# Performance work log

Hardware: AMD Instinct MI355X
Metric: run time of the kernel (lower is better)

The kernel has to match this reference:

```python
import jax, jax.numpy as jnp
import numpy as np

H = 16        # num_attention_heads
DH = 64       # attention_head_dim
D = H * DH    # model dim = 1024
FF = 4 * D    # feed-forward inner dim = 4096
SCALE = DH ** -0.5
EPS = 1e-12


def _ln(x, g, b):
    m = jnp.mean(x, axis=-1, keepdims=True)
    v = jnp.mean((x - m) ** 2, axis=-1, keepdims=True)
    return (x - m) * jax.lax.rsqrt(v + EPS) * g + b


def _attn(x, ctx, Wq, Wk, Wv, Wo, bo, mask):
    # x: [B,S,D] (already pre-normed), ctx: [B,T,D], mask: [B,T] int (1=keep) or None
    B, S, _ = x.shape
    T = ctx.shape[1]
    q = (x @ Wq).reshape(B, S, H, DH)
    k = (ctx @ Wk).reshape(B, T, H, DH)
    v = (ctx @ Wv).reshape(B, T, H, DH)
    scores = jnp.einsum('bqhd,bkhd->bhqk', q, k) * SCALE  # [B,H,S,T]
    if mask is not None:
        scores = jnp.where(mask[:, None, None, :] == 0, -jnp.inf, scores)
    probs = jax.nn.softmax(scores, axis=-1)
    out = jnp.einsum('bhqk,bkhd->bqhd', probs, v).reshape(B, S, D)
    return out @ Wo + bo


def _geglu_ff(x, Wff1, bff1, Wff2, bff2):
    y = x @ Wff1 + bff1                 # [B,S,2*FF]
    h, gate = y[..., :FF], y[..., FF:]
    # GEGLU computes exact (erf) gelu in fp32
    g = jax.nn.gelu(gate.astype(jnp.float32), approximate=False).astype(gate.dtype)
    return (h * g) @ Wff2 + bff2


def setup_inputs() -> dict:
    key = jax.random.key(0)
    ks = jax.random.split(key, 24)
    B, S, T = 4, 1024, 1024
    w = lambda k, shp: jax.random.normal(k, shp, dtype=jnp.float32) * 0.02
    inp = {
        'hidden_states': jax.random.normal(ks[0], (B, S, D), dtype=jnp.float32),
        'context': jax.random.normal(ks[1], (B, T, D), dtype=jnp.float32),
        'encoder_key_padding_mask': jnp.ones((B, T), dtype=jnp.int32),
        'g1': jnp.ones((D,), jnp.float32), 'b1': jnp.zeros((D,), jnp.float32),
        'g2': jnp.ones((D,), jnp.float32), 'b2': jnp.zeros((D,), jnp.float32),
        'g3': jnp.ones((D,), jnp.float32), 'b3': jnp.zeros((D,), jnp.float32),
        'Wq1': w(ks[2], (D, D)), 'Wk1': w(ks[3], (D, D)), 'Wv1': w(ks[4], (D, D)),
        'Wo1': w(ks[5], (D, D)), 'bo1': jnp.zeros((D,), jnp.float32),
        'Wq2': w(ks[6], (D, D)), 'Wk2': w(ks[7], (D, D)), 'Wv2': w(ks[8], (D, D)),
        'Wo2': w(ks[9], (D, D)), 'bo2': jnp.zeros((D,), jnp.float32),
        'Wff1': w(ks[10], (D, 2 * FF)), 'bff1': jnp.zeros((2 * FF,), jnp.float32),
        'Wff2': w(ks[11], (FF, D)), 'bff2': jnp.zeros((D,), jnp.float32),
    }
    return inp


def reference(hidden_states, context, encoder_key_padding_mask,
              g1, b1, g2, b2, g3, b3,
              Wq1, Wk1, Wv1, Wo1, bo1,
              Wq2, Wk2, Wv2, Wo2, bo2,
              Wff1, bff1, Wff2, bff2):
    # Self-attention (attn1): context defaults to (normed) hidden_states, no padding mask
    n1 = _ln(hidden_states, g1, b1)
    h = hidden_states + _attn(n1, n1, Wq1, Wk1, Wv1, Wo1, bo1, None)
    # Cross-attention (attn2) with encoder key padding mask
    n2 = _ln(h, g2, b2)
    h = h + _attn(n2, context, Wq2, Wk2, Wv2, Wo2, bo2, encoder_key_padding_mask)
    # GEGLU feed-forward
    h = h + _geglu_ff(_ln(h, g3, b3), Wff1, bff1, Wff2, bff2)
    return h
```

## Files before the change

kernel.cpp:

```cpp
#include <hip/hip_runtime.h>

typedef unsigned short u16;
typedef unsigned int u32;

#define B_ 4
#define S_ 1024
#define D_ 1024
#define H_ 16
#define DH_ 64
#define FF_ 4096
#define M_ 4096
#define SCALE_ 0.125f

typedef __attribute__((ext_vector_type(8))) __bf16 bf16x8;
typedef __attribute__((ext_vector_type(4))) float f32x4;

__device__ __forceinline__ f32x4 mfma16(bf16x8 a, bf16x8 b, f32x4 c) {
  return __builtin_amdgcn_mfma_f32_16x16x32_bf16(a, b, c, 0, 0, 0);
}

__device__ __forceinline__ u16 f2bf(float x) {
  union { __bf16 h; u16 u; } cv; cv.h = (__bf16)x; return cv.u;
}
__device__ __forceinline__ float bf2f(u16 u) {
  union { u32 u; float f; } cv; cv.u = ((u32)u) << 16; return cv.f;
}
__device__ __forceinline__ u32 packbf2(float a, float b) {
  union { u32 u; __bf16 h[2]; } pk;
  pk.h[0] = (__bf16)a; pk.h[1] = (__bf16)b;
  return pk.u;
}
__device__ __forceinline__ float gelu_exact(float x) {
  return 0.5f * x * (1.f + erff(x * 0.7071067811865475f));
}
__device__ __forceinline__ void gload16(const void* g, void* l) {
  __builtin_amdgcn_global_load_lds((__attribute__((address_space(1))) void*)(g),
                                   (__attribute__((address_space(3))) void*)(l),
                                   16, 0, 0);
}

template<int EPI>
__global__ __launch_bounds__(256, 2) void gemm128(
    const u16* __restrict__ A, const u16* __restrict__ BT,
    const float* __restrict__ bias, const float* __restrict__ res,
    const u16* __restrict__ aux, void* __restrict__ out,
    int M, int N, int K, int ktiles)
{
  __shared__ u16 As[2][128 * 64];
  __shared__ u16 Bs[2][128 * 64];

  const int tid = threadIdx.x;
  const int wave = tid >> 6, lane = tid & 63;
  const int wm = wave >> 1, wn = wave & 1;
  const int qi = lane & 15, g = lane >> 4;

  const int gx = N >> 7;
  const int nwg = gx * (M >> 7);
  int id = blockIdx.y * gridDim.x + blockIdx.x;
  id = (id & 7) * (nwg >> 3) + (id >> 3);
  const int m0 = (id / gx) << 7, n0 = (id % gx) << 7;

  const int NT = ktiles;
  const int kbase = blockIdx.z * ktiles * 64;

  const int r0 = tid >> 3;
  const int scol = (((tid & 7) ^ ((tid >> 3) & 7)) << 3);
  const int swb = wave << 6;

  f32x4 acc[4][4];
#pragma unroll
  for (int i = 0; i < 4; ++i)
#pragma unroll
    for (int j = 0; j < 4; ++j)
      acc[i][j] = (f32x4){0.f, 0.f, 0.f, 0.f};

#define STAGE_A(t, h, b) {                                                  \
    const int tt = (t) >= NT ? (t) - NT : (t);                              \
    _Pragma("unroll")                                                       \
    for (int i = 0; i < 2; ++i) {                                           \
      const int r = (h) * 64 + i * 32 + r0;                                 \
      gload16(A + (size_t)(m0 + r) * K + kbase + tt * 64 + scol,            \
              &As[b][(h) * 4096 + (i * 256 + swb) * 8]);                    \
    } }
#define STAGE_B(t, h, b) {                                                  \
    const int tt = (t) >= NT ? (t) - NT : (t);                              \
    _Pragma("unroll")                                                       \
    for (int i = 0; i < 2; ++i) {                                           \
      const int r = (h) * 64 + i * 32 + r0;                                 \
      gload16(BT + (size_t)(n0 + r) * K + kbase + tt * 64 + scol,           \
              &Bs[b][(h) * 4096 + (i * 256 + swb) * 8]);                    \
    } }

  bf16x8 af[4][2], bfr[4][2];

#define RD_ALL(b)                                                            \
  _Pragma("unroll") for (int mi = 0; mi < 4; ++mi)                           \
  _Pragma("unroll") for (int kk = 0; kk < 2; ++kk) {                         \
    const int row = wm * 64 + mi * 16 + qi;                                  \
    const int cb = ((kk * 64 + (g << 4)) ^ ((qi & 7) << 4));                 \
    af[mi][kk] = *(const bf16x8*)((const char*)&As[b][0] + row * 128 + cb);  \
  }                                                                          \
  _Pragma("unroll") for (int ni = 0; ni < 4; ++ni)                           \
  _Pragma("unroll") for (int kk = 0; kk < 2; ++kk) {                         \
    const int row = wn * 64 + ni * 16 + qi;                                  \
    const int cb = ((kk * 64 + (g << 4)) ^ ((qi & 7) << 4));                 \
    bfr[ni][kk] = *(const bf16x8*)((const char*)&Bs[b][0] + row * 128 + cb); \
  }

#define HALF(milo)                                                           \
  _Pragma("unroll") for (int mi = (milo); mi < (milo) + 2; ++mi)             \
  _Pragma("unroll") for (int ni = 0; ni < 4; ++ni)                           \
  _Pragma("unroll") for (int kk = 0; kk < 2; ++kk)                           \
    acc[mi][ni] = mfma16(af[mi][kk], bfr[ni][kk], acc[mi][ni]);

#define BAR() __builtin_amdgcn_s_barrier()
#define LGKM0() { asm volatile("s_waitcnt lgkmcnt(0)" ::: "memory");         \
                  __builtin_amdgcn_sched_barrier(0); }
#define VM8() asm volatile("s_waitcnt vmcnt(8)" ::: "memory")
#define PRIO(x) __builtin_amdgcn_s_setprio(x)

  STAGE_A(0, 0, 0); STAGE_A(0, 1, 0); STAGE_B(0, 0, 0); STAGE_B(0, 1, 0);
  STAGE_A(1, 0, 1); STAGE_A(1, 1, 1); STAGE_B(1, 0, 1); STAGE_B(1, 1, 1);
  VM8();
  BAR();

  const int NI = NT >> 1;
  for (int it = 0; it < NI; ++it) {
    const int k = it * 2;
    RD_ALL(0); LGKM0();
    BAR();
    STAGE_A(k + 2, 0, 0); STAGE_A(k + 2, 1, 0);
    PRIO(1); HALF(0); PRIO(0);
    STAGE_B(k + 2, 0, 0); STAGE_B(k + 2, 1, 0);
    PRIO(1); HALF(2); PRIO(0);
    VM8();
    BAR();
    RD_ALL(1); LGKM0();
    BAR();
    STAGE_A(k + 3, 0, 1); STAGE_A(k + 3, 1, 1);
    PRIO(1); HALF(0); PRIO(0);
    STAGE_B(k + 3, 0, 1); STAGE_B(k + 3, 1, 1);
    PRIO(1); HALF(2); PRIO(0);
    VM8();
    BAR();
  }

#pragma unroll
  for (int mi = 0; mi < 4; ++mi) {
#pragma unroll
    for (int ni = 0; ni < 4; ++ni) {
#pragma unroll
      for (int r = 0; r < 4; ++r) {
        const int m = m0 + wm * 64 + mi * 16 + g * 4 + r;
        const int n = n0 + wn * 64 + ni * 16 + qi;
        float v = acc[mi][ni][r];
        if (EPI == 0 || EPI == 5) {
          const int ts = n >> 10, b = m >> 10, s = m & 1023;
          const int hh = (n >> 6) & 15, dh = n & 63;
          if (EPI == 0 && ts == 0) v *= SCALE_;
          ((u16*)out)[(size_t)ts * (B_ * H_ * S_ * DH_) +
                      (((size_t)(b * H_ + hh) * S_) + s) * DH_ + dh] = f2bf(v);
        } else if (EPI == 1) {
          const size_t idx = (size_t)m * N + n;
          ((float*)out)[idx] = res[idx] + v + bias[n];
        } else if (EPI == 2) {
          ((u16*)out)[(size_t)m * N + n] = f2bf(gelu_exact(v + bias[n]));
        } else if (EPI == 3) {
          const size_t idx = (size_t)m * N + n;
          ((u16*)out)[idx] = f2bf((v + bias[n]) * bf2f(aux[idx]));
        } else {
          const size_t idx = (size_t)blockIdx.z * ((size_t)M * N) +
                             (size_t)m * N + n;
          ((u16*)out)[idx] = f2bf(v);
        }
      }
    }
  }
#undef STAGE_A
#undef STAGE_B
#undef RD_ALL
#undef HALF
#undef BAR
#undef LGKM0
#undef VM8
#undef PRIO
}

template<bool DOLN, int NS>
__global__ __launch_bounds__(256) void reduce_ln(
    const u16* __restrict__ p, const float* __restrict__ bias,
    const float* __restrict__ res, float* __restrict__ outf,
    const float* __restrict__ gg, const float* __restrict__ bb,
    u16* __restrict__ outn)
{
  __shared__ float red[8];
  const int row = blockIdx.x, tid = threadIdx.x;
  const size_t base = (size_t)row * 1024 + tid * 4;
  const size_t total = (size_t)M_ * 1024;
  float a0 = 0.f, a1 = 0.f, a2 = 0.f, a3 = 0.f;
#pragma unroll
  for (int s = 0; s < NS; ++s) {
    const uint2 u = *(const uint2*)&p[(size_t)s * total + base];
    a0 += bf2f((u16)(u.x & 0xffff));
    a1 += bf2f((u16)(u.x >> 16));
    a2 += bf2f((u16)(u.y & 0xffff));
    a3 += bf2f((u16)(u.y >> 16));
  }
  const float4 b4 = ((const float4*)bias)[tid];
  const float4 r4 = *(const float4*)&res[base];
  float4 o;
  o.x = r4.x + a0 + b4.x;
  o.y = r4.y + a1 + b4.y;
  o.z = r4.z + a2 + b4.z;
  o.w = r4.w + a3 + b4.w;
  *(float4*)&outf[base] = o;

  if (DOLN) {
    float s1 = o.x + o.y + o.z + o.w;
    float s2 = o.x * o.x + o.y * o.y + o.z * o.z + o.w * o.w;
#pragma unroll
    for (int m = 32; m; m >>= 1) {
      s1 += __shfl_xor(s1, m);
      s2 += __shfl_xor(s2, m);
    }
    const int wave = tid >> 6, lane = tid & 63;
    if (lane == 0) { red[wave * 2] = s1; red[wave * 2 + 1] = s2; }
    __syncthreads();
    const float St = red[0] + red[2] + red[4] + red[6];
    const float SQt = red[1] + red[3] + red[5] + red[7];
    const float mean = St * (1.f / 1024.f);
    float var = SQt * (1.f / 1024.f) - mean * mean;
    var = fmaxf(var, 0.f);
    const float rinv = rsqrtf(var + 1e-12f);
    const float4 g4 = ((const float4*)gg)[tid];
    const float4 bb4 = ((const float4*)bb)[tid];
    uint2 w;
    w.x = packbf2((o.x - mean) * rinv * g4.x + bb4.x,
                  (o.y - mean) * rinv * g4.y + bb4.y);
    w.y = packbf2((o.z - mean) * rinv * g4.z + bb4.z,
                  (o.w - mean) * rinv * g4.w + bb4.w);
    ((uint2*)(outn + (size_t)row * 1024))[tid] = w;
  }
}

template<int NS, bool QSC>
__global__ __launch_bounds__(256) void reduce_perm(
    const u16* __restrict__ p, u16* __restrict__ out, int M, int N)
{
  const size_t flat = ((size_t)blockIdx.x * 256 + threadIdx.x) * 4;
  const size_t total = (size_t)M * N;
  float a0 = 0.f, a1 = 0.f, a2 = 0.f, a3 = 0.f;
#pragma unroll
  for (int s = 0; s < NS; ++s) {
    const uint2 u = *(const uint2*)&p[(size_t)s * total + flat];
    a0 += bf2f((u16)(u.x & 0xffff));
    a1 += bf2f((u16)(u.x >> 16));
    a2 += bf2f((u16)(u.y & 0xffff));
    a3 += bf2f((u16)(u.y >> 16));
  }
  if (QSC) { a0 *= SCALE_; a1 *= SCALE_; a2 *= SCALE_; a3 *= SCALE_; }
  const int m = (int)(flat / N), nb = (int)(flat % N);
  const int ts = nb >> 10, hh = (nb >> 6) & 15, dh = nb & 63;
  const int b = m >> 10, sI = m & 1023;
  uint2 w;
  w.x = packbf2(a0, a1);
  w.y = packbf2(a2, a3);
  *(uint2*)&out[(size_t)ts * (B_ * H_ * S_ * DH_) +
                (((size_t)(b * H_ + hh) * S_) + sI) * DH_ + dh] = w;
}

template<bool MASKED>
__global__ __launch_bounds__(256, 4) void attn_kernel(
    const u16* __restrict__ Q, const u16* __restrict__ Kb,
    const u16* __restrict__ VT, const float* __restrict__ bias,
    u16* __restrict__ O, int S, int T)
{
  __shared__ u16 Ks[64 * 72];
  __shared__ u16 VTs[64 * 72];
  __shared__ u16 Ps[4][16 * 72];
  __shared__ float biasS[64];

  const int bh = blockIdx.y;
  const int b = bh >> 4, h = bh & 15;
  const int tid = threadIdx.x;
  const int wave = tid >> 6, lane = tid & 63;
  const int g = lane >> 4, qi = lane & 15;
  const int q0w = blockIdx.x * 64 + wave * 16;

  const u16* Qb = Q + (size_t)bh * S * DH_;
  const u16* Kg = Kb + (size_t)bh * T * DH_;
  const u16* Vg = VT + (size_t)bh * DH_ * T;

  bf16x8 qf[2];
  qf[0] = *(const bf16x8*)&Qb[(q0w + qi) * DH_ + g * 8];
  qf[1] = *(const bf16x8*)&Qb[(q0w + qi) * DH_ + 32 + g * 8];

  f32x4 acc[4];
#pragma unroll
  for (int i = 0; i < 4; ++i) acc[i] = (f32x4){0.f, 0.f, 0.f, 0.f};
  float l_run = 1e-30f;

  u16* Pw = &Ps[wave][0];

  for (int t0 = 0; t0 < T; t0 += 64) {
    __syncthreads();
#pragma unroll
    for (int i = 0; i < 2; ++i) {
      const int flat = i * 256 + tid;
      const int row = flat >> 3, kc = flat & 7;
      *(uint4*)&Ks[row * 72 + kc * 8] = *(const uint4*)&Kg[(size_t)(t0 + row) * DH_ + kc * 8];
      *(uint4*)&VTs[row * 72 + kc * 8] = *(const uint4*)&Vg[(size_t)row * T + t0 + kc * 8];
    }
    if (MASKED && tid < 64) biasS[tid] = bias[b * T + t0 + tid];
    __syncthreads();

    f32x4 sacc[4];
#pragma unroll
    for (int nt = 0; nt < 4; ++nt) sacc[nt] = (f32x4){0.f, 0.f, 0.f, 0.f};
#pragma unroll
    for (int kk = 0; kk < 2; ++kk) {
#pragma unroll
      for (int nt = 0; nt < 4; ++nt) {
        bf16x8 kf = *(const bf16x8*)&Ks[(nt * 16 + qi) * 72 + kk * 32 + g * 8];
        sacc[nt] = mfma16(kf, qf[kk], sacc[nt]);
      }
    }
    float p[4][4];
    float lsum = 0.f;
#pragma unroll
    for (int nt = 0; nt < 4; ++nt)
#pragma unroll
      for (int r = 0; r < 4; ++r) {
        float v = sacc[nt][r];
        if (MASKED) v += biasS[nt * 16 + g * 4 + r];
        const float e = __expf(v);
        p[nt][r] = e;
        lsum += e;
      }
    lsum += __shfl_xor(lsum, 16);
    lsum += __shfl_xor(lsum, 32);
    l_run += lsum;

#pragma unroll
    for (int nt = 0; nt < 4; ++nt) {
      uint2 w;
      w.x = packbf2(p[nt][0], p[nt][1]);
      w.y = packbf2(p[nt][2], p[nt][3]);
      *(uint2*)&Pw[qi * 72 + nt * 16 + g * 4] = w;
    }

#pragma unroll
    for (int kk = 0; kk < 2; ++kk) {
      bf16x8 pf = *(const bf16x8*)&Pw[qi * 72 + kk * 32 + g * 8];
#pragma unroll
      for (int ndh = 0; ndh < 4; ++ndh) {
        bf16x8 vf = *(const bf16x8*)&VTs[(ndh * 16 + qi) * 72 + kk * 32 + g * 8];
        acc[ndh] = mfma16(vf, pf, acc[ndh]);
      }
    }
  }

  const float inv = 1.f / l_run;
  const int qg = q0w + qi;
#pragma unroll
  for (int ndh = 0; ndh < 4; ++ndh) {
    uint2 w;
    w.x = packbf2(acc[ndh][0] * inv, acc[ndh][1] * inv);
    w.y = packbf2(acc[ndh][2] * inv, acc[ndh][3] * inv);
    *(uint2*)&O[(size_t)(b * S_ + qg) * D_ + h * DH_ + ndh * 16 + g * 4] = w;
  }
}

__global__ __launch_bounds__(256) void ln_kernel(
    const float* __restrict__ x, const float* __restrict__ gg,
    const float* __restrict__ bb, u16* __restrict__ out)
{
  __shared__ float red[8];
  const int row = blockIdx.x, tid = threadIdx.x;
  const float4 v = ((const float4*)(x + (size_t)row * D_))[tid];
  float s = v.x + v.y + v.z + v.w;
  float sq = v.x * v.x + v.y * v.y + v.z * v.z + v.w * v.w;
#pragma unroll
  for (int m = 32; m; m >>= 1) {
    s += __shfl_xor(s, m);
    sq += __shfl_xor(sq, m);
  }
  const int wave = tid >> 6, lane = tid & 63;
  if (lane == 0) { red[wave * 2] = s; red[wave * 2 + 1] = sq; }
  __syncthreads();
  const float St = red[0] + red[2] + red[4] + red[6];
  const float SQt = red[1] + red[3] + red[5] + red[7];
  const float mean = St * (1.f / 1024.f);
  float var = SQt * (1.f / 1024.f) - mean * mean;
  var = fmaxf(var, 0.f);
  const float rinv = rsqrtf(var + 1e-12f);
  const float4 g4 = ((const float4*)gg)[tid];
  const float4 b4 = ((const float4*)bb)[tid];
  uint2 o;
  o.x = packbf2((v.x - mean) * rinv * g4.x + b4.x, (v.y - mean) * rinv * g4.y + b4.y);
  o.y = packbf2((v.z - mean) * rinv * g4.z + b4.z, (v.w - mean) * rinv * g4.w + b4.w);
  ((uint2*)(out + (size_t)row * D_))[tid] = o;
}

__global__ __launch_bounds__(256) void transpose_w(
    const float* __restrict__ in, u16* __restrict__ out, int K, int N)
{
  __shared__ float tile[32][33];
  const int tx = threadIdx.x & 31, ty = threadIdx.x >> 5;
  const int k0 = blockIdx.y * 32, n0 = blockIdx.x * 32;
#pragma unroll
  for (int j = 0; j < 4; ++j)
    tile[ty + 8 * j][tx] = in[(size_t)(k0 + ty + 8 * j) * N + n0 + tx];
  __syncthreads();
#pragma unroll
  for (int j = 0; j < 4; ++j)
    out[(size_t)(n0 + ty + 8 * j) * K + k0 + tx] = f2bf(tile[tx][ty + 8 * j]);
}

__global__ __launch_bounds__(256) void transpose_v(
    const u16* __restrict__ in, u16* __restrict__ out, int T)
{
  __shared__ u16 tile[32][33];
  const int tx = threadIdx.x & 31, ty = threadIdx.x >> 5;
  const int bh = blockIdx.z;
  const int t0 = blockIdx.x * 32, d0 = blockIdx.y * 32;
  const u16* ib = in + (size_t)bh * T * DH_;
  u16* ob = out + (size_t)bh * DH_ * T;
#pragma unroll
  for (int j = 0; j < 4; ++j)
    tile[ty + 8 * j][tx] = ib[(size_t)(t0 + ty + 8 * j) * DH_ + d0 + tx];
  __syncthreads();
#pragma unroll
  for (int j = 0; j < 4; ++j)
    ob[(size_t)(d0 + ty + 8 * j) * T + t0 + tx] = tile[tx][ty + 8 * j];
}

__global__ void cvt_bf16(const float* __restrict__ in, u16* __restrict__ out, int n4)
{
  const int i = blockIdx.x * blockDim.x + threadIdx.x;
  if (i < n4) {
    const float4 v = ((const float4*)in)[i];
    uint2 o;
    o.x = packbf2(v.x, v.y);
    o.y = packbf2(v.z, v.w);
    ((uint2*)out)[i] = o;
  }
}

__global__ void mask_bias(const int* __restrict__ mask, float* __restrict__ bias, int n)
{
  const int i = blockIdx.x * blockDim.x + threadIdx.x;
  if (i < n) bias[i] = mask[i] ? 0.f : -1e30f;
}

extern "C" void kernel_launch(void* const* d_in, const int* in_sizes, int n_in,
                              void* d_out, int out_size, void* d_ws, size_t ws_size,
                              hipStream_t stream)
{
  (void)in_sizes; (void)n_in; (void)out_size; (void)ws_size;
  const float* hidden = (const float*)d_in[0];
  const float* ctx    = (const float*)d_in[1];
  const int*   mask   = (const int*)d_in[2];
  const float* g1 = (const float*)d_in[3];
  const float* b1 = (const float*)d_in[4];
  const float* g2 = (const float*)d_in[5];
  const float* b2 = (const float*)d_in[6];
  const float* g3 = (const float*)d_in[7];
  const float* b3 = (const float*)d_in[8];
  const float* Wq1 = (const float*)d_in[9];
  const float* Wk1 = (const float*)d_in[10];
  const float* Wv1 = (const float*)d_in[11];
  const float* Wo1 = (const float*)d_in[12];
  const float* bo1 = (const float*)d_in[13];
  const float* Wq2 = (const float*)d_in[14];
  const float* Wk2 = (const float*)d_in[15];
  const float* Wv2 = (const float*)d_in[16];
  const float* Wo2 = (const float*)d_in[17];
  const float* bo2 = (const float*)d_in[18];
  const float* Wff1 = (const float*)d_in[19];
  const float* bff1 = (const float*)d_in[20];
  const float* Wff2 = (const float*)d_in[21];
  const float* bff2 = (const float*)d_in[22];

  char* ws = (char*)d_ws;
  size_t off = 0;
  auto alloc = [&](size_t bytes) -> void* {
    void* p = ws + off;
    off += (bytes + 255) & ~(size_t)255;
    return p;
  };
  u16* WqT1  = (u16*)alloc((size_t)1024 * 1024 * 2);
  u16* WkT1  = (u16*)alloc((size_t)1024 * 1024 * 2);
  u16* WvT1  = (u16*)alloc((size_t)1024 * 1024 * 2);
  u16* WoT1  = (u16*)alloc((size_t)1024 * 1024 * 2);
  u16* WqT2  = (u16*)alloc((size_t)1024 * 1024 * 2);
  u16* WkT2  = (u16*)alloc((size_t)1024 * 1024 * 2);
  u16* WvT2  = (u16*)alloc((size_t)1024 * 1024 * 2);
  u16* WoT2  = (u16*)alloc((size_t)1024 * 1024 * 2);
  u16* Wff1T = (u16*)alloc((size_t)8192 * 1024 * 2);
  u16* Wff2T = (u16*)alloc((size_t)1024 * 4096 * 2);
  u16* nbuf  = (u16*)alloc((size_t)M_ * D_ * 2);
  u16* hgbuf = (u16*)alloc((size_t)M_ * FF_ * 2);
  u16* qbuf  = (u16*)alloc((size_t)M_ * D_ * 2);
  u16* kbuf  = (u16*)alloc((size_t)M_ * D_ * 2);
  u16* vbuf  = (u16*)alloc((size_t)M_ * D_ * 2);
  u16* vtbuf = (u16*)alloc((size_t)M_ * D_ * 2);
  u16* attnb = (u16*)alloc((size_t)M_ * D_ * 2);
  u16* ctxb  = (u16*)alloc((size_t)M_ * D_ * 2);
  u16* pbuf  = (u16*)alloc((size_t)4 * M_ * D_ * 2);
  float* biasw = (float*)alloc((size_t)B_ * S_ * 4);
  u16* gbuf = qbuf;
  float* hres = (float*)d_out;

  const dim3 blk(256);
  const dim3 gW(32, 32);
  const dim3 gQKV(24, 32);
  const dim3 gKV(16, 32);
  const dim3 gFF(32, 32);
  const dim3 gS2(8, 32, 2);
  const dim3 gF2(8, 32, 4);
  const dim3 gA(16, 64);
  const dim3 gV(32, 2, 64);
  const dim3 gR(4096);

  transpose_w<<<gW, blk, 0, stream>>>(Wq1, WqT1, 1024, 1024);
  transpose_w<<<gW, blk, 0, stream>>>(Wk1, WkT1, 1024, 1024);
  transpose_w<<<gW, blk, 0, stream>>>(Wv1, WvT1, 1024, 1024);
  transpose_w<<<gW, blk, 0, stream>>>(Wo1, WoT1, 1024, 1024);
  transpose_w<<<gW, blk, 0, stream>>>(Wq2, WqT2, 1024, 1024);
  transpose_w<<<gW, blk, 0, stream>>>(Wk2, WkT2, 1024, 1024);
  transpose_w<<<gW, blk, 0, stream>>>(Wv2, WvT2, 1024, 1024);
  transpose_w<<<gW, blk, 0, stream>>>(Wo2, WoT2, 1024, 1024);
  transpose_w<<<dim3(256, 32), blk, 0, stream>>>(Wff1, Wff1T, 1024, 8192);
  transpose_w<<<dim3(32, 128), blk, 0, stream>>>(Wff2, Wff2T, 4096, 1024);
  cvt_bf16<<<dim3((1048576 + 255) / 256), blk, 0, stream>>>(ctx, ctxb, 1048576);
  mask_bias<<<dim3(16), blk, 0, stream>>>(mask, biasw, B_ * S_);

  ln_kernel<<<dim3(M_), blk, 0, stream>>>(hidden, g1, b1, nbuf);
  gemm128<0><<<gQKV, blk, 0, stream>>>(nbuf, WqT1, nullptr, nullptr, nullptr,
                                       qbuf, M_, 3072, 1024, 16);
  transpose_v<<<gV, blk, 0, stream>>>(vbuf, vtbuf, 1024);
  attn_kernel<false><<<gA, blk, 0, stream>>>(qbuf, kbuf, vtbuf, nullptr, attnb, S_, S_);
  gemm128<4><<<gS2, blk, 0, stream>>>(attnb, WoT1, nullptr, nullptr, nullptr,
                                      pbuf, M_, 1024, 1024, 8);
  reduce_ln<true, 2><<<gR, blk, 0, stream>>>(pbuf, bo1, hidden, hres, g2, b2, nbuf);

  gemm128<4><<<gS2, blk, 0, stream>>>(nbuf, WqT2, nullptr, nullptr, nullptr,
                                      pbuf, M_, 1024, 1024, 8);
  reduce_perm<2, true><<<gR, blk, 0, stream>>>(pbuf, qbuf, M_, 1024);
  gemm128<5><<<gKV, blk, 0, stream>>>(ctxb, WkT2, nullptr, nullptr, nullptr,
                                      kbuf, M_, 2048, 1024, 16);
  transpose_v<<<gV, blk, 0, stream>>>(vbuf, vtbuf, 1024);
  attn_kernel<true><<<gA, blk, 0, stream>>>(qbuf, kbuf, vtbuf, biasw, attnb, S_, S_);
  gemm128<4><<<gS2, blk, 0, stream>>>(attnb, WoT2, nullptr, nullptr, nullptr,
                                      pbuf, M_, 1024, 1024, 8);
  reduce_ln<true, 2><<<gR, blk, 0, stream>>>(pbuf, bo2, hres, hres, g3, b3, nbuf);

  gemm128<2><<<gFF, blk, 0, stream>>>(nbuf, Wff1T + (size_t)FF_ * 1024, bff1 + FF_,
                                      nullptr, nullptr, gbuf, M_, FF_, 1024, 16);
  gemm128<3><<<gFF, blk, 0, stream>>>(nbuf, Wff1T, bff1, nullptr, gbuf, hgbuf,
                                      M_, FF_, 1024, 16);
  gemm128<4><<<gF2, blk, 0, stream>>>(hgbuf, Wff2T, nullptr, nullptr, nullptr,
                                      pbuf, M_, 1024, 4096, 16);
  reduce_ln<false, 4><<<gR, blk, 0, stream>>>(pbuf, bff2, hres, hres, nullptr,
                                              nullptr, nullptr);
}
```

Before: 404.9 us.

## Add 256x256-tile 512-thread GEMM for feed-forward projections

Introduces a new GEMM kernel with 256x256 output tiles, 8 waves per block, double-buffered swizzled LDS staging and interleaved MFMA halves with load issue. The three feed-forward GEMMs (gate with GELU, value times gate, and the split-K down projection) switch from the 128-tile kernel to it. Larger tiles raise arithmetic intensity and cut global reloads of A and B, but use 128 KB of LDS per block and many accumulator registers, which lowers occupancy and reduces the number of blocks (256 for the up projections, 256 for split-K down).

```diff
diff --git a/kernel.cpp b/kernel.cpp
--- a/kernel.cpp
+++ b/kernel.cpp
@@ -180,6 +180,135 @@
 #undef STAGE_B
 #undef RD_ALL
 #undef HALF
+#undef BAR
+#undef LGKM0
+#undef VM8
+#undef PRIO
+}
+
+template<int EPI>
+__global__ __launch_bounds__(512, 2) void gemm256b(
+    const u16* __restrict__ A, const u16* __restrict__ BT,
+    const float* __restrict__ bias, const float* __restrict__ res,
+    const u16* __restrict__ aux, void* __restrict__ out,
+    int M, int N, int K, int ktiles)
+{
+  __shared__ u16 As[2][256 * 64];
+  __shared__ u16 Bs[2][256 * 64];
+
+  const int tid = threadIdx.x;
+  const int wave = tid >> 6, lane = tid & 63;
+  const int wm = wave >> 2, wn = wave & 3;
+  const int qi = lane & 15, g = lane >> 4;
+
+  const int gx = N >> 8;
+  const int nwg = gx * (M >> 8);
+  int id = blockIdx.y * gridDim.x + blockIdx.x;
+  id = (id & 7) * (nwg >> 3) + (id >> 3);
+  const int m0 = (id / gx) << 8, n0 = (id % gx) << 8;
+
+  const int NT = ktiles;
+  const int kbase = blockIdx.z * ktiles * 64;
+
+  const int srow = tid >> 3;
+  const int scol = (((tid & 7) ^ ((tid >> 3) & 7)) << 3);
+  const int sldsb = wave << 9;
+
+  f32x4 acc[8][4];
+#pragma unroll
+  for (int i = 0; i < 8; ++i)
+#pragma unroll
+    for (int j = 0; j < 4; ++j)
+      acc[i][j] = (f32x4){0.f, 0.f, 0.f, 0.f};
+
+#define STAGE_A(t, b) {                                                     \
+    const int tt = (t) >= NT ? (t) - NT : (t);                              \
+    _Pragma("unroll")                                                       \
+    for (int i = 0; i < 4; ++i) {                                           \
+      const int r = i * 64 + srow;                                          \
+      gload16(A + (size_t)(m0 + r) * K + kbase + tt * 64 + scol,            \
+              &As[b][i * 4096 + sldsb]);                                    \
+    } }
+#define STAGE_B(t, b) {                                                     \
+    const int tt = (t) >= NT ? (t) - NT : (t);                              \
+    _Pragma("unroll")                                                       \
+    for (int i = 0; i < 4; ++i) {                                           \
+      const int r = i * 64 + srow;                                          \
+      gload16(BT + (size_t)(n0 + r) * K + kbase + tt * 64 + scol,           \
+              &Bs[b][i * 4096 + sldsb]);                                    \
+    } }
+
+  bf16x8 af[8][2], bfr[4][2];
+
+#define RD_ALL(b)                                                            \
+  _Pragma("unroll") for (int mi = 0; mi < 8; ++mi)                           \
+  _Pragma("unroll") for (int kk = 0; kk < 2; ++kk) {                         \
+    const int row = wm * 128 + mi * 16 + qi;                                 \
+    const int cb = ((kk * 64 + (g << 4)) ^ ((qi & 7) << 4));                 \
+    af[mi][kk] = *(const bf16x8*)((const char*)&As[b][0] + row * 128 + cb);  \
+  }                                                                          \
+  _Pragma("unroll") for (int ni = 0; ni < 4; ++ni)                           \
+  _Pragma("unroll") for (int kk = 0; kk < 2; ++kk) {                         \
+    const int row = wn * 64 + ni * 16 + qi;                                  \
+    const int cb = ((kk * 64 + (g << 4)) ^ ((qi & 7) << 4));                 \
+    bfr[ni][kk] = *(const bf16x8*)((const char*)&Bs[b][0] + row * 128 + cb); \
+  }
+
+#define MHALF(milo)                                                          \
+  _Pragma("unroll") for (int mi = (milo); mi < (milo) + 4; ++mi)             \
+  _Pragma("unroll") for (int ni = 0; ni < 4; ++ni)                           \
+  _Pragma("unroll") for (int kk = 0; kk < 2; ++kk)                           \
+    acc[mi][ni] = mfma16(af[mi][kk], bfr[ni][kk], acc[mi][ni]);
+
+#define BAR() __builtin_amdgcn_s_barrier()
+#define LGKM0() { asm volatile("s_waitcnt lgkmcnt(0)" ::: "memory");         \
+                  __builtin_amdgcn_sched_barrier(0); }
+#define VM8() asm volatile("s_waitcnt vmcnt(8)" ::: "memory")
+#define PRIO(x) __builtin_amdgcn_s_setprio(x)
+
+  STAGE_A(0, 0); STAGE_B(0, 0);
+  STAGE_A(1, 1); STAGE_B(1, 1);
+  VM8();
+  BAR();
+
+  for (int t = 0; t < NT; ++t) {
+    const int b = t & 1;
+    RD_ALL(b); LGKM0();
+    BAR();
+    STAGE_A(t + 2, b);
+    PRIO(1); MHALF(0); PRIO(0);
+    STAGE_B(t + 2, b);
+    PRIO(1); MHALF(4); PRIO(0);
+    VM8();
+    BAR();
+  }
+
+#pragma unroll
+  for (int mi = 0; mi < 8; ++mi) {
+#pragma unroll
+    for (int ni = 0; ni < 4; ++ni) {
+#pragma unroll
+      for (int r = 0; r < 4; ++r) {
+        const int m = m0 + wm * 128 + mi * 16 + g * 4 + r;
+        const int n = n0 + wn * 64 + ni * 16 + qi;
+        const float v = acc[mi][ni][r];
+        if (EPI == 2) {
+          ((u16*)out)[(size_t)m * N + n] = f2bf(gelu_exact(v + bias[n]));
+        } else if (EPI == 3) {
+          const size_t idx = (size_t)m * N + n;
+          ((u16*)out)[idx] = f2bf((v + bias[n]) * bf2f(aux[idx]));
+        } else {
+          const size_t idx = (size_t)blockIdx.z * ((size_t)M * N) +
+                             (size_t)m * N + n;
+          ((u16*)out)[idx] = f2bf(v);
+        }
+      }
+    }
+  }
+#undef STAGE_A
+#undef STAGE_B
+#undef RD_ALL
+#undef MHALF
 #undef BAR
 #undef LGKM0
 #undef VM8
@@ -513,12 +642,13 @@
   float* hres = (float*)d_out;
 
   const dim3 blk(256);
+  const dim3 blk512(512);
   const dim3 gW(32, 32);
   const dim3 gQKV(24, 32);
   const dim3 gKV(16, 32);
-  const dim3 gFF(32, 32);
+  const dim3 gFFb(16, 16);
+  const dim3 gF2b(4, 16, 4);
   const dim3 gS2(8, 32, 2);
-  const dim3 gF2(8, 32, 4);
   const dim3 gA(16, 64);
   const dim3 gV(32, 2, 64);
   const dim3 gR(4096);
@@ -556,12 +686,13 @@
                                       pbuf, M_, 1024, 1024, 8);
   reduce_ln<true, 2><<<gR, blk, 0, stream>>>(pbuf, bo2, hres, hres, g3, b3, nbuf);
 
-  gemm128<2><<<gFF, blk, 0, stream>>>(nbuf, Wff1T + (size_t)FF_ * 1024, bff1 + FF_,
-                                      nullptr, nullptr, gbuf, M_, FF_, 1024, 16);
-  gemm128<3><<<gFF, blk, 0, stream>>>(nbuf, Wff1T, bff1, nullptr, gbuf, hgbuf,
-                                      M_, FF_, 1024, 16);
-  gemm128<4><<<gF2, blk, 0, stream>>>(hgbuf, Wff2T, nullptr, nullptr, nullptr,
-                                      pbuf, M_, 1024, 4096, 16);
+  gemm256b<2><<<gFFb, blk512, 0, stream>>>(nbuf, Wff1T + (size_t)FF_ * 1024,
+                                           bff1 + FF_, nullptr, nullptr, gbuf,
+                                           M_, FF_, 1024, 16);
+  gemm256b<3><<<gFFb, blk512, 0, stream>>>(nbuf, Wff1T, bff1, nullptr, gbuf,
+                                           hgbuf, M_, FF_, 1024, 16);
+  gemm256b<4><<<gF2b, blk512, 0, stream>>>(hgbuf, Wff2T, nullptr, nullptr, nullptr,
+                                           pbuf, M_, 1024, 4096, 16);
   reduce_ln<false, 4><<<gR, blk, 0, stream>>>(pbuf, bff2, hres, hres, nullptr,
                                               nullptr, nullptr);
 }
```

New measurement: 403.9 us. No clear change (-0.2%).

## Drop split-K partials, fuse GEGLU dual GEMM, batch weight transposes

Applied to the files above, without the earlier changes.

Split-K GEMMs that wrote bf16 partials and needed separate reduce kernels are replaced by full-K GEMMs that add bias and residual directly in the epilogue, with a plain LayerNorm kernel following. The two FF1 GEMMs (gate with GELU, then value multiply) become one kernel that computes both accumulators from a shared A tile and applies GEGLU in registers, so the intermediate gate buffer is never written. The eight 1024x1024 weight transposes are merged into one launch. The trade-offs: the N=1024 GEMMs now launch only 256 workgroups, which may underfill the GPU, and the new GEGLU kernel is single-buffered and holds twice the accumulators, which raises register pressure.

```diff
diff --git a/kernel.cpp b/kernel.cpp
--- a/kernel.cpp
+++ b/kernel.cpp
@@ -43,8 +43,7 @@
 __global__ __launch_bounds__(256, 2) void gemm128(
     const u16* __restrict__ A, const u16* __restrict__ BT,
     const float* __restrict__ bias, const float* __restrict__ res,
-    const u16* __restrict__ aux, void* __restrict__ out,
-    int M, int N, int K, int ktiles)
+    void* __restrict__ out, int M, int N, int K, int ktiles)
 {
   __shared__ u16 As[2][128 * 64];
   __shared__ u16 Bs[2][128 * 64];
@@ -160,18 +159,9 @@
           if (EPI == 0 && ts == 0) v *= SCALE_;
           ((u16*)out)[(size_t)ts * (B_ * H_ * S_ * DH_) +
                       (((size_t)(b * H_ + hh) * S_) + s) * DH_ + dh] = f2bf(v);
-        } else if (EPI == 1) {
+        } else {
           const size_t idx = (size_t)m * N + n;
           ((float*)out)[idx] = res[idx] + v + bias[n];
-        } else if (EPI == 2) {
-          ((u16*)out)[(size_t)m * N + n] = f2bf(gelu_exact(v + bias[n]));
-        } else if (EPI == 3) {
-          const size_t idx = (size_t)m * N + n;
-          ((u16*)out)[idx] = f2bf((v + bias[n]) * bf2f(aux[idx]));
-        } else {
-          const size_t idx = (size_t)blockIdx.z * ((size_t)M * N) +
-                             (size_t)m * N + n;
-          ((u16*)out)[idx] = f2bf(v);
         }
       }
     }
@@ -186,87 +176,117 @@
 #undef PRIO
 }
 
-template<bool DOLN, int NS>
-__global__ __launch_bounds__(256) void reduce_ln(
-    const u16* __restrict__ p, const float* __restrict__ bias,
-    const float* __restrict__ res, float* __restrict__ outf,
-    const float* __restrict__ gg, const float* __restrict__ bb,
-    u16* __restrict__ outn)
-{
-  __shared__ float red[8];
-  const int row = blockIdx.x, tid = threadIdx.x;
-  const size_t base = (size_t)row * 1024 + tid * 4;
-  const size_t total = (size_t)M_ * 1024;
-  float a0 = 0.f, a1 = 0.f, a2 = 0.f, a3 = 0.f;
-#pragma unroll
-  for (int s = 0; s < NS; ++s) {
-    const uint2 u = *(const uint2*)&p[(size_t)s * total + base];
-    a0 += bf2f((u16)(u.x & 0xffff));
-    a1 += bf2f((u16)(u.x >> 16));
-    a2 += bf2f((u16)(u.y & 0xffff));
-    a3 += bf2f((u16)(u.y >> 16));
-  }
-  const float4 b4 = ((const float4*)bias)[tid];
-  const float4 r4 = *(const float4*)&res[base];
-  float4 o;
-  o.x = r4.x + a0 + b4.x;
-  o.y = r4.y + a1 + b4.y;
-  o.z = r4.z + a2 + b4.z;
-  o.w = r4.w + a3 + b4.w;
-  *(float4*)&outf[base] = o;
-
-  if (DOLN) {
-    float s1 = o.x + o.y + o.z + o.w;
-    float s2 = o.x * o.x + o.y * o.y + o.z * o.z + o.w * o.w;
-#pragma unroll
-    for (int m = 32; m; m >>= 1) {
-      s1 += __shfl_xor(s1, m);
-      s2 += __shfl_xor(s2, m);
-    }
-    const int wave = tid >> 6, lane = tid & 63;
-    if (lane == 0) { red[wave * 2] = s1; red[wave * 2 + 1] = s2; }
+__global__ __launch_bounds__(256, 2) void ffgeglu(
+    const u16* __restrict__ A, const u16* __restrict__ BTh,
+    const u16* __restrict__ BTg, const float* __restrict__ bias,
+    u16* __restrict__ out)
+{
+  __shared__ u16 As[128 * 64];
+  __shared__ u16 Bhs[128 * 64];
+  __shared__ u16 Bgs[128 * 64];
+
+  const int tid = threadIdx.x;
+  const int wave = tid >> 6, lane = tid & 63;
+  const int wm = wave >> 1, wn = wave & 1;
+  const int qi = lane & 15, g = lane >> 4;
+
+  const int gx = 32;
+  const int nwg = 1024;
+  int id = blockIdx.y * gridDim.x + blockIdx.x;
+  id = (id & 7) * (nwg >> 3) + (id >> 3);
+  const int m0 = (id / gx) << 7, n0 = (id % gx) << 7;
+  const int K = 1024;
+
+  const int r0 = tid >> 3;
+  const int scol = (((tid & 7) ^ ((tid >> 3) & 7)) << 3);
+  const int swb = wave << 6;
+
+  f32x4 acch[4][4], accg[4][4];
+#pragma unroll
+  for (int i = 0; i < 4; ++i)
+#pragma unroll
+    for (int j = 0; j < 4; ++j) {
+      acch[i][j] = (f32x4){0.f, 0.f, 0.f, 0.f};
+      accg[i][j] = (f32x4){0.f, 0.f, 0.f, 0.f};
+    }
+
+  for (int t = 0; t < 16; ++t) {
+    if (t) __syncthreads();
+#pragma unroll
+    for (int i = 0; i < 4; ++i) {
+      const int r = i * 32 + r0;
+      gload16(A + (size_t)(m0 + r) * K + t * 64 + scol,
+              &As[(i * 256 + swb) * 8]);
+    }
+#pragma unroll
+    for (int i = 0; i < 4; ++i) {
+      const int r = i * 32 + r0;
+      gload16(BTh + (size_t)(n0 + r) * K + t * 64 + scol,
+              &Bhs[(i * 256 + swb) * 8]);
+    }
+#pragma unroll
+    for (int i = 0; i < 4; ++i) {
+      const int r = i * 32 + r0;
+      gload16(BTg + (size_t)(n0 + r) * K + t * 64 + scol,
+              &Bgs[(i * 256 + swb) * 8]);
+    }
     __syncthreads();
-    const float St = red[0] + red[2] + red[4] + red[6];
-    const float SQt = red[1] + red[3] + red[5] + red[7];
-    const float mean = St * (1.f / 1024.f);
-    float var = SQt * (1.f / 1024.f) - mean * mean;
-    var = fmaxf(var, 0.f);
-    const float rinv = rsqrtf(var + 1e-12f);
-    const float4 g4 = ((const float4*)gg)[tid];
-    const float4 bb4 = ((const float4*)bb)[tid];
-    uint2 w;
-    w.x = packbf2((o.x - mean) * rinv * g4.x + bb4.x,
-                  (o.y - mean) * rinv * g4.y + bb4.y);
-    w.y = packbf2((o.z - mean) * rinv * g4.z + bb4.z,
-                  (o.w - mean) * rinv * g4.w + bb4.w);
-    ((uint2*)(outn + (size_t)row * 1024))[tid] = w;
-  }
-}
-
-template<int NS, bool QSC>
-__global__ __launch_bounds__(256) void reduce_perm(
-    const u16* __restrict__ p, u16* __restrict__ out, int M, int N)
-{
-  const size_t flat = ((size_t)blockIdx.x * 256 + threadIdx.x) * 4;
-  const size_t total = (size_t)M * N;
-  float a0 = 0.f, a1 = 0.f, a2 = 0.f, a3 = 0.f;
-#pragma unroll
-  for (int s = 0; s < NS; ++s) {
-    const uint2 u = *(const uint2*)&p[(size_t)s * total + flat];
-    a0 += bf2f((u16)(u.x & 0xffff));
-    a1 += bf2f((u16)(u.x >> 16));
-    a2 += bf2f((u16)(u.y & 0xffff));
-    a3 += bf2f((u16)(u.y >> 16));
-  }
-  if (QSC) { a0 *= SCALE_; a1 *= SCALE_; a2 *= SCALE_; a3 *= SCALE_; }
-  const int m = (int)(flat / N), nb = (int)(flat % N);
-  const int ts = nb >> 10, hh = (nb >> 6) & 15, dh = nb & 63;
-  const int b = m >> 10, sI = m & 1023;
-  uint2 w;
-  w.x = packbf2(a0, a1);
-  w.y = packbf2(a2, a3);
-  *(uint2*)&out[(size_t)ts * (B_ * H_ * S_ * DH_) +
-                (((size_t)(b * H_ + hh) * S_) + sI) * DH_ + dh] = w;
+
+    bf16x8 af[4][2], bfr[4][2];
+#pragma unroll
+    for (int mi = 0; mi < 4; ++mi)
+#pragma unroll
+      for (int kk = 0; kk < 2; ++kk) {
+        const int row = wm * 64 + mi * 16 + qi;
+        const int cb = ((kk * 64 + (g << 4)) ^ ((qi & 7) << 4));
+        af[mi][kk] = *(const bf16x8*)((const char*)&As[0] + row * 128 + cb);
+      }
+#pragma unroll
+    for (int ni = 0; ni < 4; ++ni)
+#pragma unroll
+      for (int kk = 0; kk < 2; ++kk) {
+        const int row = wn * 64 + ni * 16 + qi;
+        const int cb = ((kk * 64 + (g << 4)) ^ ((qi & 7) << 4));
+        bfr[ni][kk] = *(const bf16x8*)((const char*)&Bhs[0] + row * 128 + cb);
+      }
+#pragma unroll
+    for (int mi = 0; mi < 4; ++mi)
+#pragma unroll
+      for (int ni = 0; ni < 4; ++ni)
+#pragma unroll
+        for (int kk = 0; kk < 2; ++kk)
+          acch[mi][ni] = mfma16(af[mi][kk], bfr[ni][kk], acch[mi][ni]);
+#pragma unroll
+    for (int ni = 0; ni < 4; ++ni)
+#pragma unroll
+      for (int kk = 0; kk < 2; ++kk) {
+        const int row = wn * 64 + ni * 16 + qi;
+        const int cb = ((kk * 64 + (g << 4)) ^ ((qi & 7) << 4));
+        bfr[ni][kk] = *(const bf16x8*)((const char*)&Bgs[0] + row * 128 + cb);
+      }
+#pragma unroll
+    for (int mi = 0; mi < 4; ++mi)
+#pragma unroll
+      for (int ni = 0; ni < 4; ++ni)
+#pragma unroll
+        for (int kk = 0; kk < 2; ++kk)
+          accg[mi][ni] = mfma16(af[mi][kk], bfr[ni][kk], accg[mi][ni]);
+  }
+
+#pragma unroll
+  for (int mi = 0; mi < 4; ++mi) {
+#pragma unroll
+    for (int ni = 0; ni < 4; ++ni) {
+#pragma unroll
+      for (int r = 0; r < 4; ++r) {
+        const int m = m0 + wm * 64 + mi * 16 + g * 4 + r;
+        const int n = n0 + wn * 64 + ni * 16 + qi;
+        const float hv = acch[mi][ni][r] + bias[n];
+        const float gv = accg[mi][ni][r] + bias[FF_ + n];
+        out[(size_t)m * FF_ + n] = f2bf(hv * gelu_exact(gv));
+      }
+    }
+  }
 }
 
 template<bool MASKED>
@@ -415,6 +435,28 @@
 #pragma unroll
   for (int j = 0; j < 4; ++j)
     out[(size_t)(n0 + ty + 8 * j) * K + k0 + tx] = f2bf(tile[tx][ty + 8 * j]);
+}
+
+__global__ __launch_bounds__(256) void transpose_w8(
+    const float* __restrict__ w0, const float* __restrict__ w1,
+    const float* __restrict__ w2, const float* __restrict__ w3,
+    const float* __restrict__ w4, const float* __restrict__ w5,
+    const float* __restrict__ w6, const float* __restrict__ w7,
+    u16* __restrict__ outbase)
+{
+  __shared__ float tile[32][33];
+  const float* srcs[8] = {w0, w1, w2, w3, w4, w5, w6, w7};
+  const float* in = srcs[blockIdx.z];
+  u16* out = outbase + (size_t)blockIdx.z * 1024 * 1024;
+  const int tx = threadIdx.x & 31, ty = threadIdx.x >> 5;
+  const int k0 = blockIdx.y * 32, n0 = blockIdx.x * 32;
+#pragma unroll
+  for (int j = 0; j < 4; ++j)
+    tile[ty + 8 * j][tx] = in[(size_t)(k0 + ty + 8 * j) * 1024 + n0 + tx];
+  __syncthreads();
+#pragma unroll
+  for (int j = 0; j < 4; ++j)
+    out[(size_t)(n0 + ty + 8 * j) * 1024 + k0 + tx] = f2bf(tile[tx][ty + 8 * j]);
 }
 
 __global__ __launch_bounds__(256) void transpose_v(
@@ -507,61 +549,49 @@
   u16* vtbuf = (u16*)alloc((size_t)M_ * D_ * 2);
   u16* attnb = (u16*)alloc((size_t)M_ * D_ * 2);
   u16* ctxb  = (u16*)alloc((size_t)M_ * D_ * 2);
-  u16* pbuf  = (u16*)alloc((size_t)4 * M_ * D_ * 2);
   float* biasw = (float*)alloc((size_t)B_ * S_ * 4);
-  u16* gbuf = qbuf;
   float* hres = (float*)d_out;
+  (void)WkT1; (void)WvT1; (void)WkT2; (void)WvT2; (void)WoT2;
 
   const dim3 blk(256);
-  const dim3 gW(32, 32);
+  const dim3 gW8(32, 32, 8);
   const dim3 gQKV(24, 32);
   const dim3 gKV(16, 32);
+  const dim3 gP(8, 32);
   const dim3 gFF(32, 32);
-  const dim3 gS2(8, 32, 2);
-  const dim3 gF2(8, 32, 4);
   const dim3 gA(16, 64);
   const dim3 gV(32, 2, 64);
-  const dim3 gR(4096);
-
-  transpose_w<<<gW, blk, 0, stream>>>(Wq1, WqT1, 1024, 1024);
-  transpose_w<<<gW, blk, 0, stream>>>(Wk1, WkT1, 1024, 1024);
-  transpose_w<<<gW, blk, 0, stream>>>(Wv1, WvT1, 1024, 1024);
-  transpose_w<<<gW, blk, 0, stream>>>(Wo1, WoT1, 1024, 1024);
-  transpose_w<<<gW, blk, 0, stream>>>(Wq2, WqT2, 1024, 1024);
-  transpose_w<<<gW, blk, 0, stream>>>(Wk2, WkT2, 1024, 1024);
-  transpose_w<<<gW, blk, 0, stream>>>(Wv2, WvT2, 1024, 1024);
-  transpose_w<<<gW, blk, 0, stream>>>(Wo2, WoT2, 1024, 1024);
+
+  transpose_w8<<<gW8, blk, 0, stream>>>(Wq1, Wk1, Wv1, Wo1, Wq2, Wk2, Wv2, Wo2,
+                                        WqT1);
   transpose_w<<<dim3(256, 32), blk, 0, stream>>>(Wff1, Wff1T, 1024, 8192);
   transpose_w<<<dim3(32, 128), blk, 0, stream>>>(Wff2, Wff2T, 4096, 1024);
-  cvt_bf16<<<dim3((1048576 + 255) / 256), blk, 0, stream>>>(ctx, ctxb, 1048576);
+  cvt_bf16<<<dim3(4096), blk, 0, stream>>>(ctx, ctxb, 1048576);
   mask_bias<<<dim3(16), blk, 0, stream>>>(mask, biasw, B_ * S_);
 
   ln_kernel<<<dim3(M_), blk, 0, stream>>>(hidden, g1, b1, nbuf);
-  gemm128<0><<<gQKV, blk, 0, stream>>>(nbuf, WqT1, nullptr, nullptr, nullptr,
+  gemm128<0><<<gQKV, blk, 0, stream>>>(nbuf, WqT1, nullptr, nullptr,
                                        qbuf, M_, 3072, 1024, 16);
   transpose_v<<<gV, blk, 0, stream>>>(vbuf, vtbuf, 1024);
-  attn_kernel<false><<<gA, blk, 0, stream>>>(qbuf, kbuf, vtbuf, nullptr, attnb, S_, S_);
-  gemm128<4><<<gS2, blk, 0, stream>>>(attnb, WoT1, nullptr, nullptr, nullptr,
-                                      pbuf, M_, 1024, 1024, 8);
-  reduce_ln<true, 2><<<gR, blk, 0, stream>>>(pbuf, bo1, hidden, hres, g2, b2, nbuf);
-
-  gemm128<4><<<gS2, blk, 0, stream>>>(nbuf, WqT2, nullptr, nullptr, nullptr,
-                                      pbuf, M_, 1024, 1024, 8);
-  reduce_perm<2, true><<<gR, blk, 0, stream>>>(pbuf, qbuf, M_, 1024);
-  gemm128<5><<<gKV, blk, 0, stream>>>(ctxb, WkT2, nullptr, nullptr, nullptr,
+  attn_kernel<false><<<gA, blk, 0, stream>>>(qbuf, kbuf, vtbuf, nullptr, attnb,
+                                             S_, S_);
+  gemm128<1><<<gP, blk, 0, stream>>>(attnb, WoT1, bo1, hidden,
+                                     hres, M_, 1024, 1024, 16);
+  ln_kernel<<<dim3(M_), blk, 0, stream>>>(hres, g2, b2, nbuf);
+
+  gemm128<0><<<gP, blk, 0, stream>>>(nbuf, WqT2, nullptr, nullptr,
+                                     qbuf, M_, 1024, 1024, 16);
+  gemm128<5><<<gKV, blk, 0, stream>>>(ctxb, WkT2, nullptr, nullptr,
                                       kbuf, M_, 2048, 1024, 16);
   transpose_v<<<gV, blk, 0, stream>>>(vbuf, vtbuf, 1024);
-  attn_kernel<true><<<gA, blk, 0, stream>>>(qbuf, kbuf, vtbuf, biasw, attnb, S_, S_);
-  gemm128<4><<<gS2, blk, 0, stream>>>(attnb, WoT2, nullptr, nullptr, nullptr,
-                                      pbuf, M_, 1024, 1024, 8);
-  reduce_ln<true, 2><<<gR, blk, 0, stream>>>(pbuf, bo2, hres, hres, g3, b3, nbuf);
-
-  gemm128<2><<<gFF, blk, 0, stream>>>(nbuf, Wff1T + (size_t)FF_ * 1024, bff1 + FF_,
-                                      nullptr, nullptr, gbuf, M_, FF_, 1024, 16);
-  gemm128<3><<<gFF, blk, 0, stream>>>(nbuf, Wff1T, bff1, nullptr, gbuf, hgbuf,
-                                      M_, FF_, 1024, 16);
-  gemm128<4><<<gF2, blk, 0, stream>>>(hgbuf, Wff2T, nullptr, nullptr, nullptr,
-                                      pbuf, M_, 1024, 4096, 16);
-  reduce_ln<false, 4><<<gR, blk, 0, stream>>>(pbuf, bff2, hres, hres, nullptr,
-                                              nullptr, nullptr);
-}
+  attn_kernel<true><<<gA, blk, 0, stream>>>(qbuf, kbuf, vtbuf, biasw, attnb,
+                                            S_, S_);
+  gemm128<1><<<gP, blk, 0, stream>>>(attnb, WoT2, bo2, hres,
+                                     hres, M_, 1024, 1024, 16);
+  ln_kernel<<<dim3(M_), blk, 0, stream>>>(hres, g3, b3, nbuf);
+
+  ffgeglu<<<gFF, blk, 0, stream>>>(nbuf, Wff1T, Wff1T + (size_t)FF_ * 1024,
+                                   bff1, hgbuf);
+  gemm128<1><<<gP, blk, 0, stream>>>(hgbuf, Wff2T, bff2, hres,
+                                     hres, M_, 1024, 4096, 64);
+}
```

After: 361.4 us. 1.12x faster.
